# Kernel tuning notes

Hardware: AMD Instinct MI355X
Metric: run time of the kernel (lower is better)

Reference implementation:

```python
import jax, jax.numpy as jnp
import numpy as np

VOCAB = 21128; EMBED = 768; D_MODEL = 256; H = 100; NTAGS = 21; B = 32; T = 256


def setup_inputs() -> dict:
    key = jax.random.key(0)
    ks = jax.random.split(key, 18)
    n = lambda k, s, sc=0.05: jax.random.normal(k, s, dtype=jnp.float32) * sc
    return {
        "words": jax.random.randint(ks[0], (B, T), 0, VOCAB),
        "target": jax.random.randint(ks[1], (B, T), 0, NTAGS),
        "embed_table": n(ks[2], (VOCAB, EMBED), 1.0),
        "in_fc_w": n(ks[3], (D_MODEL, EMBED)),
        "in_fc_b": n(ks[4], (D_MODEL,)),
        "Wih0": n(ks[5], (2, 4 * H, D_MODEL)),
        "Whh0": n(ks[6], (2, 4 * H, H)),
        "bih0": n(ks[7], (2, 4 * H)),
        "bhh0": n(ks[8], (2, 4 * H)),
        "Wih1": n(ks[9], (2, 4 * H, 2 * H)),
        "Whh1": n(ks[10], (2, 4 * H, H)),
        "bih1": n(ks[11], (2, 4 * H)),
        "bhh1": n(ks[12], (2, 4 * H)),
        "out_w": n(ks[13], (NTAGS, 2 * H)),
        "out_b": n(ks[14], (NTAGS,)),
        "trans": n(ks[15], (NTAGS, NTAGS)),
        "start_s": n(ks[16], (NTAGS,)),
        "end_s": n(ks[17], (NTAGS,)),
    }


def _lstm_dir(x, Wih, Whh, bih, bhh, reverse):
    # x: (T, B, D); torch LSTM gate order i, f, g, o
    Bsz, Hd = x.shape[1], Whh.shape[1]
    pre = jnp.einsum('tbd,gd->tbg', x, Wih) + bih  # precompute input projection

    def step(carry, p):
        h, c = carry
        g = p + h @ Whh.T + bhh
        i, f, gg, o = jnp.split(g, 4, axis=-1)
        c = jax.nn.sigmoid(f) * c + jax.nn.sigmoid(i) * jnp.tanh(gg)
        h = jax.nn.sigmoid(o) * jnp.tanh(c)
        return (h, c), h

    init = (jnp.zeros((Bsz, Hd), x.dtype), jnp.zeros((Bsz, Hd), x.dtype))
    _, hs = jax.lax.scan(step, init, pre, reverse=reverse)
    return hs


def _bilstm(x, layers):
    h = x
    for (Wih, Whh, bih, bhh) in layers:  # fixed small loop over num_layers
        f = _lstm_dir(h, Wih[0], Whh[0], bih[0], bhh[0], False)
        b = _lstm_dir(h, Wih[1], Whh[1], bih[1], bhh[1], True)
        h = jnp.concatenate([f, b], axis=-1)
    return h


def _crf_loss(logits, tags, mask, trans, start_s, end_s):
    # fastNLP ConditionalRandomField loss: normalizer - gold_score, per batch elem
    lt = jnp.swapaxes(logits, 0, 1)          # (T, B, N)
    tt = tags.T                               # (T, B)
    mt = mask.T.astype(logits.dtype)          # (T, B)
    alpha0 = lt[0] + start_s

    def step(alpha, inp):
        emit, m = inp
        tmp = alpha[:, :, None] + trans[None] + emit[:, None, :]  # (B, N, N)
        new = jax.nn.logsumexp(tmp, axis=1)
        return jnp.where(m[:, None] > 0, new, alpha), None

    alpha, _ = jax.lax.scan(step, alpha0, (lt[1:], mt[1:]))
    normalizer = jax.nn.logsumexp(alpha + end_s, axis=1)  # (B,)

    emit_sc = jnp.take_along_axis(lt, tt[..., None], axis=2)[..., 0] * mt
    trans_sc = trans[tt[:-1], tt[1:]] * mt[1:]
    seq_lens = mask.sum(axis=1)
    last_idx = jnp.maximum(seq_lens - 1, 0)
    last_tags = tags[jnp.arange(tags.shape[0]), last_idx]
    gold = emit_sc.sum(0) + trans_sc.sum(0) + start_s[tt[0]] + end_s[last_tags]
    return normalizer - gold


def reference(words, target, embed_table, in_fc_w, in_fc_b, Wih0, Whh0, bih0, bhh0,
              Wih1, Whh1, bih1, bhh1, out_w, out_b, trans, start_s, end_s):
    mask = words != 0
    x = embed_table[words]                       # (B, T, E)
    x = x @ in_fc_w.T + in_fc_b                  # (B, T, D)
    x = jnp.swapaxes(x, 0, 1)                    # (T, B, D)
    h = _bilstm(x, [(Wih0, Whh0, bih0, bhh0), (Wih1, Whh1, bih1, bhh1)])
    h = jnp.swapaxes(h, 0, 1)                    # (B, T, 2H); dropout is identity at eval
    logits = jax.nn.log_softmax(h @ out_w.T + out_b, axis=-1)
    return _crf_loss(logits, target, mask, trans, start_s, end_s)  # (B,)
```

## Files before the change

### kernel.cpp

```cpp
#include <hip/hip_runtime.h>
#include <hip/hip_bf16.h>

#define VOCAB 21128
#define EMBED 768
#define DMODEL 256
#define HID 100
#define NTAGS 21
#define BB 32
#define TT 256
#define NTOK (BB*TT)

typedef float f32x4 __attribute__((ext_vector_type(4)));
typedef unsigned int u32x4 __attribute__((ext_vector_type(4)));
typedef short s16x8 __attribute__((ext_vector_type(8)));

__device__ __forceinline__ float sigm(float x) { return 1.0f / (1.0f + __expf(-x)); }
__device__ __forceinline__ float tanh_(float x) { return 2.0f / (1.0f + __expf(-2.0f * x)) - 1.0f; }

__device__ __forceinline__ unsigned int bfr(float x) {
    unsigned int u = __float_as_uint(x);
    return (u + 0x7fffu + ((u >> 16) & 1u)) >> 16;
}
__device__ __forceinline__ unsigned int bfpack(float lo, float hi) {
    return (bfr(hi) << 16) | bfr(lo);
}
__device__ __forceinline__ s16x8 asfrag(u32x4 v) {
    union { u32x4 u; s16x8 s; } x; x.u = v; return x.s;
}

__global__ __launch_bounds__(256) void gemm_mfma(
    const float* __restrict__ A, int lda,
    const float* __restrict__ B, int ldb,
    const float* __restrict__ bias1, const float* __restrict__ bias2,
    float* __restrict__ C, int ldc,
    int N, int K,
    const int* __restrict__ gatherWords, int permGates)
{
    __shared__ unsigned int As_[2][2048];
    __shared__ unsigned int Bs_[2][1024];

    const int tid = threadIdx.x;
    const int row0 = blockIdx.x * 128;
    const int col0 = blockIdx.y * 64;
    const int lane = tid & 63;
    const int wave = tid >> 6;
    const int wr = wave >> 1, wc = wave & 1;
    const int nsteps = (K + 31) >> 5;

    const float* arow[4]; int aoff[4]; int kqA[4];
    #pragma unroll
    for (int j = 0; j < 4; ++j) {
        int v = tid + 256 * j;
        int row = v >> 3, kq = v & 7;
        int grow = row0 + row;
        const float* ap;
        if (gatherWords) {
            int widx = gatherWords[(grow & 31) * TT + (grow >> 5)];
            ap = A + (size_t)widx * lda;
        } else {
            ap = A + (size_t)grow * lda;
        }
        arow[j] = ap + 4 * kq;
        aoff[j] = (row >> 4) * 256 + (kq >> 1) * 64 + (row & 15) * 4 + (kq & 1) * 2;
        kqA[j] = kq;
    }
    const float* brow[2]; int boff[2]; int bok[2]; int kqB[2];
    #pragma unroll
    for (int j = 0; j < 2; ++j) {
        int v = tid + 256 * j;
        int r = v >> 3, kq = v & 7;
        int gcol = col0 + r;
        bok[j] = (gcol < N);
        int src = bok[j] ? gcol : 0;
        if (permGates && bok[j]) {
            int d2 = (gcol >= 400) ? 1 : 0;
            int rr = gcol - d2 * 400;
            src = d2 * 400 + (rr & 3) * 100 + (rr >> 2);
        }
        brow[j] = B + (size_t)src * ldb + 4 * kq;
        boff[j] = (r >> 4) * 256 + (kq >> 1) * 64 + (r & 15) * 4 + (kq & 1) * 2;
        kqB[j] = kq;
    }

    {
        #pragma unroll
        for (int j = 0; j < 4; ++j) {
            f32x4 v = {0.f,0.f,0.f,0.f};
            if (4 * kqA[j] < K) v = *(const f32x4*)(arow[j]);
            As_[0][aoff[j]]     = bfpack(v.x, v.y);
            As_[0][aoff[j] + 1] = bfpack(v.z, v.w);
        }
        #pragma unroll
        for (int j = 0; j < 2; ++j) {
            f32x4 v = {0.f,0.f,0.f,0.f};
            if (bok[j] && 4 * kqB[j] < K) v = *(const f32x4*)(brow[j]);
            Bs_[0][boff[j]]     = bfpack(v.x, v.y);
            Bs_[0][boff[j] + 1] = bfpack(v.z, v.w);
        }
    }
    __syncthreads();

    f32x4 acc[4][2] = {};

    for (int s = 0; s < nsteps; ++s) {
        const int cur = s & 1, nxt = cur ^ 1;

        f32x4 la[4], lb[2];
        if (s + 1 < nsteps) {
            const int kb = (s + 1) * 32;
            #pragma unroll
            for (int j = 0; j < 4; ++j) {
                la[j] = (f32x4){0.f,0.f,0.f,0.f};
                if (kb + 4 * kqA[j] < K) la[j] = *(const f32x4*)(arow[j] + kb);
            }
            #pragma unroll
            for (int j = 0; j < 2; ++j) {
                lb[j] = (f32x4){0.f,0.f,0.f,0.f};
                if (bok[j] && kb + 4 * kqB[j] < K) lb[j] = *(const f32x4*)(brow[j] + kb);
            }
        }

        u32x4 af[4], bf[2];
        #pragma unroll
        for (int mt = 0; mt < 4; ++mt)
            af[mt] = *(const u32x4*)&As_[cur][(4 * wr + mt) * 256 + lane * 4];
        #pragma unroll
        for (int nt = 0; nt < 2; ++nt)
            bf[nt] = *(const u32x4*)&Bs_[cur][(2 * wc + nt) * 256 + lane * 4];
        #pragma unroll
        for (int mt = 0; mt < 4; ++mt)
            #pragma unroll
            for (int nt = 0; nt < 2; ++nt)
                acc[mt][nt] = __builtin_amdgcn_mfma_f32_16x16x32_bf16(
                    asfrag(af[mt]), asfrag(bf[nt]), acc[mt][nt], 0, 0, 0);

        if (s + 1 < nsteps) {
            #pragma unroll
            for (int j = 0; j < 4; ++j) {
                As_[nxt][aoff[j]]     = bfpack(la[j].x, la[j].y);
                As_[nxt][aoff[j] + 1] = bfpack(la[j].z, la[j].w);
            }
            #pragma unroll
            for (int j = 0; j < 2; ++j) {
                Bs_[nxt][boff[j]]     = bfpack(lb[j].x, lb[j].y);
                Bs_[nxt][boff[j] + 1] = bfpack(lb[j].z, lb[j].w);
            }
        }
        __syncthreads();
    }

    const int r4 = (lane >> 4) * 4;
    const int cl = lane & 15;
    #pragma unroll
    for (int nt = 0; nt < 2; ++nt) {
        int gcol = col0 + (2 * wc + nt) * 16 + cl;
        if (gcol < N) {
            int src = gcol;
            if (permGates) {
                int d2 = (gcol >= 400) ? 1 : 0;
                int rr = gcol - d2 * 400;
                src = d2 * 400 + (rr & 3) * 100 + (rr >> 2);
            }
            float bv = bias1[src];
            if (bias2) bv += bias2[src];
            #pragma unroll
            for (int mt = 0; mt < 4; ++mt) {
                int grow = row0 + (4 * wr + mt) * 16 + r4;
                #pragma unroll
                for (int r = 0; r < 4; ++r)
                    C[(size_t)(grow + r) * ldc + gcol] = acc[mt][nt][r] + bv;
            }
        }
    }
}

#define STASH_FRAG(DD, F, A0,A1,A2,A3) { \
    int tile = 4*wave + DD; if (tile > 24) tile = 24; \
    int row16 = 16*tile + m16; \
    const float* srcp = Whh + (size_t)(dir*400 + (row16 & 3)*100 + (row16 >> 2)) * HID; \
    const int k0 = 32*F + 8*g4; \
    f32x4 fa = {0.f,0.f,0.f,0.f}, fb = {0.f,0.f,0.f,0.f}; \
    if (k0 < HID) fa = *(const f32x4*)(srcp + k0); \
    if (k0 + 4 < HID) fb = *(const f32x4*)(srcp + k0 + 4); \
    unsigned p0 = bfpack(fa.x, fa.y), p1 = bfpack(fa.z, fa.w); \
    unsigned p2 = bfpack(fb.x, fb.y), p3 = bfpack(fb.z, fb.w); \
    asm volatile("v_accvgpr_write_b32 a" #A0 ", %0\n\t" \
                 "v_accvgpr_write_b32 a" #A1 ", %1\n\t" \
                 "v_accvgpr_write_b32 a" #A2 ", %2\n\t" \
                 "v_accvgpr_write_b32 a" #A3 ", %3" \
                 :: "v"(p0), "v"(p1), "v"(p2), "v"(p3) \
                 : "a" #A0, "a" #A1, "a" #A2, "a" #A3); }

#define MF(ACC, BF, A0, A3) \
    asm volatile("v_mfma_f32_16x16x32_bf16 %0, a[" #A0 ":" #A3 "], %1, %0" \
                 : "+v"(ACC) : "v"(BF));

#define LSTM_STEP(P0,P1,P2,P3, S) { \
    const int t_ = dir ? (TT-1-(S)) : (S); \
    const int i_ = t_ * BB + b; \
    const u32x4* hb_ = (const u32x4*)&h16[(S) & 1][0]; \
    u32x4 bf0 = hb_[g4], bf1 = hb_[4+g4], bf2 = hb_[8+g4], bf3 = hb_[12+g4]; \
    f32x4 acc0 = P0, acc1 = P1, acc2 = P2, acc3 = P3; \
    if ((S) + 2 < TT) { \
        const int tn_ = dir ? (TT-3-(S)) : ((S)+2); \
        const size_t ib_ = (size_t)(tn_ * BB + b) * 800; \
        P0 = *(const f32x4*)(pre + ib_ + po0); \
        P1 = *(const f32x4*)(pre + ib_ + po1); \
        P2 = *(const f32x4*)(pre + ib_ + po2); \
        P3 = *(const f32x4*)(pre + ib_ + po3); \
    } \
    asm volatile("s_nop 1"); \
    MF(acc0, bf0, 0, 3)   MF(acc1, bf0, 16, 19) MF(acc2, bf0, 32, 35) MF(acc3, bf0, 48, 51) \
    MF(acc0, bf1, 4, 7)   MF(acc1, bf1, 20, 23) MF(acc2, bf1, 36, 39) MF(acc3, bf1, 52, 55) \
    MF(acc0, bf2, 8, 11)  MF(acc1, bf2, 24, 27) MF(acc2, bf2, 40, 43) MF(acc3, bf2, 56, 59) \
    MF(acc0, bf3, 12, 15) MF(acc1, bf3, 28, 31) MF(acc2, bf3, 44, 47) MF(acc3, bf3, 60, 63) \
    asm volatile("s_nop 7\n\ts_nop 7"); \
    f32x4 sel = (d == 0) ? acc0 : (d == 1) ? acc1 : (d == 2) ? acc2 : acc3; \
    float igt = sigm(sel.x); \
    float fgt = sigm(sel.y); \
    float ggt = tanh_(sel.z); \
    float ogt = sigm(sel.w); \
    c = fgt * c + igt * ggt; \
    float h = ogt * tanh_(c); \
    if (writer) { \
        h16[((S) + 1) & 1][my_u] = (unsigned short)bfr(h); \
        hout[(size_t)i_ * 200 + dir * HID + my_u] = h; \
    } \
    __syncthreads(); }

__global__ __launch_bounds__(448, 1) void lstm_mfma(
    const float* __restrict__ pre,
    const float* __restrict__ Whh,
    float* __restrict__ hout)
{
    const int dir = blockIdx.x >> 5;
    const int b = blockIdx.x & 31;
    const int tid = threadIdx.x;
    const int wave = tid >> 6;
    const int lane = tid & 63;
    const int m16 = lane & 15;
    const int g4 = lane >> 4;
    const int d = lane & 3;

    __shared__ alignas(16) unsigned short h16[2][128];

    STASH_FRAG(0,0, 0,1,2,3)    STASH_FRAG(0,1, 4,5,6,7)
    STASH_FRAG(0,2, 8,9,10,11)  STASH_FRAG(0,3, 12,13,14,15)
    STASH_FRAG(1,0, 16,17,18,19) STASH_FRAG(1,1, 20,21,22,23)
    STASH_FRAG(1,2, 24,25,26,27) STASH_FRAG(1,3, 28,29,30,31)
    STASH_FRAG(2,0, 32,33,34,35) STASH_FRAG(2,1, 36,37,38,39)
    STASH_FRAG(2,2, 40,41,42,43) STASH_FRAG(2,3, 44,45,46,47)
    STASH_FRAG(3,0, 48,49,50,51) STASH_FRAG(3,1, 52,53,54,55)
    STASH_FRAG(3,2, 56,57,58,59) STASH_FRAG(3,3, 60,61,62,63)

    if (tid < 128) { h16[0][tid] = 0; h16[1][tid] = 0; }

    int tl0 = 4*wave + 0; if (tl0 > 24) tl0 = 24;
    int tl1 = 4*wave + 1; if (tl1 > 24) tl1 = 24;
    int tl2 = 4*wave + 2; if (tl2 > 24) tl2 = 24;
    int tl3 = 4*wave + 3; if (tl3 > 24) tl3 = 24;
    const int po0 = dir*400 + 16*tl0 + 4*g4;
    const int po1 = dir*400 + 16*tl1 + 4*g4;
    const int po2 = dir*400 + 16*tl2 + 4*g4;
    const int po3 = dir*400 + 16*tl3 + 4*g4;
    int my_tile = 4*wave + d; if (my_tile > 24) my_tile = 24;
    const int my_u = my_tile*4 + g4;
    const bool writer = ((lane & 12) == 0) && (wave < 6 || d == 0);

    float c = 0.f;
    __syncthreads();

    const size_t ib0 = (size_t)((dir ? (TT-1) : 0) * BB + b) * 800;
    const size_t ib1 = (size_t)((dir ? (TT-2) : 1) * BB + b) * 800;
    f32x4 pa0 = *(const f32x4*)(pre + ib0 + po0);
    f32x4 pa1 = *(const f32x4*)(pre + ib0 + po1);
    f32x4 pa2 = *(const f32x4*)(pre + ib0 + po2);
    f32x4 pa3 = *(const f32x4*)(pre + ib0 + po3);
    f32x4 pb0 = *(const f32x4*)(pre + ib1 + po0);
    f32x4 pb1 = *(const f32x4*)(pre + ib1 + po1);
    f32x4 pb2 = *(const f32x4*)(pre + ib1 + po2);
    f32x4 pb3 = *(const f32x4*)(pre + ib1 + po3);

    for (int s = 0; s < TT; s += 2) {
        LSTM_STEP(pa0, pa1, pa2, pa3, s)
        LSTM_STEP(pb0, pb1, pb2, pb3, s + 1)
    }
}

__global__ __launch_bounds__(256) void logits_lsm(
    const float* __restrict__ h1,
    const float* __restrict__ out_w,
    const float* __restrict__ out_b,
    float* __restrict__ logits)
{
    const int lane = threadIdx.x & 63;
    const int wid = (blockIdx.x * 256 + threadIdx.x) >> 6;
    const int half = lane >> 5;
    const int n = lane & 31;
    const int i = wid * 2 + half;
    if (i >= NTOK) return;

    float acc = -1e30f;
    if (n < NTAGS) {
        acc = out_b[n];
        const float4* hr = (const float4*)(h1 + (size_t)i * 200);
        const float4* wr = (const float4*)(out_w + (size_t)n * 200);
        #pragma unroll
        for (int e = 0; e < 50; ++e) {
            float4 h4 = hr[e], w4 = wr[e];
            acc += h4.x * w4.x + h4.y * w4.y + h4.z * w4.z + h4.w * w4.w;
        }
    }
    float m = acc;
    for (int off = 16; off > 0; off >>= 1) m = fmaxf(m, __shfl_xor(m, off, 32));
    float ex = (n < NTAGS) ? __expf(acc - m) : 0.f;
    float s = ex;
    for (int off = 16; off > 0; off >>= 1) s += __shfl_xor(s, off, 32);
    if (n < NTAGS) logits[(size_t)i * NTAGS + n] = acc - m - __logf(s);
}

__global__ __launch_bounds__(64) void crf_kernel(
    const float* __restrict__ logits,
    const int* __restrict__ words,
    const int* __restrict__ target,
    const float* __restrict__ trans,
    const float* __restrict__ start_s,
    const float* __restrict__ end_s,
    float* __restrict__ out)
{
    const int b = blockIdx.x;
    const int j = threadIdx.x;

    float tcol[NTAGS];
    #pragma unroll
    for (int i = 0; i < NTAGS; ++i) tcol[i] = (j < NTAGS) ? trans[i * NTAGS + j] : 0.f;

    float alpha = (j < NTAGS) ? (logits[(size_t)(0 * BB + b) * NTAGS + j] + start_s[j]) : -1e30f;

    for (int t = 1; t < TT; ++t) {
        bool mt = (words[b * TT + t] != 0);
        if (mt) {
            float v[NTAGS];
            float mx = -1e30f;
            #pragma unroll
            for (int i2 = 0; i2 < NTAGS; ++i2) {
                float ai = __shfl(alpha, i2, 64);
                v[i2] = ai + tcol[i2];
                mx = fmaxf(mx, v[i2]);
            }
            float s = 0.f;
            #pragma unroll
            for (int i2 = 0; i2 < NTAGS; ++i2) s += __expf(v[i2] - mx);
            float na = mx + __logf(s) + logits[(size_t)(t * BB + b) * NTAGS + j];
            alpha = (j < NTAGS) ? na : -1e30f;
        }
    }

    float val = (j < NTAGS) ? (alpha + end_s[j]) : -1e30f;
    float mx = val;
    for (int off = 32; off > 0; off >>= 1) mx = fmaxf(mx, __shfl_xor(mx, off, 64));
    float s = (j < NTAGS) ? __expf(val - mx) : 0.f;
    for (int off = 32; off > 0; off >>= 1) s += __shfl_xor(s, off, 64);
    float norm = mx + __logf(s);

    float gold = 0.f, slen = 0.f;
    for (int t = j; t < TT; t += 64) {
        int tg = target[b * TT + t];
        bool m = (words[b * TT + t] != 0);
        if (m) {
            gold += logits[(size_t)(t * BB + b) * NTAGS + tg];
            slen += 1.f;
            if (t >= 1) gold += trans[target[b * TT + t - 1] * NTAGS + tg];
        }
    }
    for (int off = 32; off > 0; off >>= 1) {
        gold += __shfl_xor(gold, off, 64);
        slen += __shfl_xor(slen, off, 64);
    }
    if (j == 0) {
        int len = (int)slen;
        int last = (len > 0) ? (len - 1) : 0;
        int last_tag = target[b * TT + last];
        gold += start_s[target[b * TT + 0]] + end_s[last_tag];
        out[b] = norm - gold;
    }
}

extern "C" void kernel_launch(void* const* d_in, const int* in_sizes, int n_in,
                              void* d_out, int out_size, void* d_ws, size_t ws_size,
                              hipStream_t stream) {
    const int*   words   = (const int*)  d_in[0];
    const int*   target  = (const int*)  d_in[1];
    const float* embed   = (const float*)d_in[2];
    const float* in_fc_w = (const float*)d_in[3];
    const float* in_fc_b = (const float*)d_in[4];
    const float* Wih0    = (const float*)d_in[5];
    const float* Whh0    = (const float*)d_in[6];
    const float* bih0    = (const float*)d_in[7];
    const float* bhh0    = (const float*)d_in[8];
    const float* Wih1    = (const float*)d_in[9];
    const float* Whh1    = (const float*)d_in[10];
    const float* bih1    = (const float*)d_in[11];
    const float* bhh1    = (const float*)d_in[12];
    const float* out_w   = (const float*)d_in[13];
    const float* out_b   = (const float*)d_in[14];
    const float* trans   = (const float*)d_in[15];
    const float* start_s = (const float*)d_in[16];
    const float* end_s   = (const float*)d_in[17];
    float* out = (float*)d_out;

    float* ws = (float*)d_ws;
    float* x      = ws;
    float* pre    = ws + 2097152;
    float* h0     = ws + 8650752;
    float* h1     = ws;
    float* logits = ws + 1638400;

    gemm_mfma<<<dim3(64, 4), 256, 0, stream>>>(
        embed, EMBED, in_fc_w, EMBED, in_fc_b, nullptr,
        x, DMODEL, DMODEL, EMBED, words, 0);

    gemm_mfma<<<dim3(64, 13), 256, 0, stream>>>(
        x, DMODEL, Wih0, DMODEL, bih0, bhh0,
        pre, 800, 800, DMODEL, nullptr, 1);

    lstm_mfma<<<64, 448, 0, stream>>>(pre, Whh0, h0);

    gemm_mfma<<<dim3(64, 13), 256, 0, stream>>>(
        h0, 200, Wih1, 200, bih1, bhh1,
        pre, 800, 800, 200, nullptr, 1);

    lstm_mfma<<<64, 448, 0, stream>>>(pre, Whh1, h1);

    logits_lsm<<<NTOK / 8, 256, 0, stream>>>(h1, out_w, out_b, logits);

    crf_kernel<<<BB, 64, 0, stream>>>(logits, words, target, trans, start_s, end_s, out);
}
```

Baseline: 619.0 us.

## Stage LSTM gate preactivations in LDS chunks and use lighter barriers

Result: faster. 580.6 us (-6.2%).

```diff
diff --git a/kernel.cpp b/kernel.cpp
--- a/kernel.cpp
+++ b/kernel.cpp
@@ -27,6 +27,12 @@
 __device__ __forceinline__ s16x8 asfrag(u32x4 v) {
     union { u32x4 u; s16x8 s; } x; x.u = v; return x.s;
 }
+
+#define BAR() do { \
+    asm volatile("s_waitcnt lgkmcnt(0)" ::: "memory"); \
+    __builtin_amdgcn_s_barrier(); \
+    __builtin_amdgcn_sched_barrier(0); \
+} while (0)
 
 __global__ __launch_bounds__(256) void gemm_mfma(
     const float* __restrict__ A, int lda,
@@ -98,7 +104,7 @@
             Bs_[0][boff[j] + 1] = bfpack(v.z, v.w);
         }
     }
-    __syncthreads();
+    BAR();
 
     f32x4 acc[4][2] = {};
 
@@ -146,7 +152,7 @@
                 Bs_[nxt][boff[j] + 1] = bfpack(lb[j].z, lb[j].w);
             }
         }
-        __syncthreads();
+        BAR();
     }
 
     const int r4 = (lane >> 4) * 4;
@@ -195,20 +201,29 @@
     asm volatile("v_mfma_f32_16x16x32_bf16 %0, a[" #A0 ":" #A3 "], %1, %0" \
                  : "+v"(ACC) : "v"(BF));
 
-#define LSTM_STEP(P0,P1,P2,P3, S) { \
-    const int t_ = dir ? (TT-1-(S)) : (S); \
-    const int i_ = t_ * BB + b; \
-    const u32x4* hb_ = (const u32x4*)&h16[(S) & 1][0]; \
+#define LOADCHUNK(K2) { \
+    const int s0_ = 16 * (K2); \
+    _Pragma("unroll") \
+    for (int j = 0; j < 4; ++j) { \
+        if (okj[j]) { \
+            int tg = dir ? (TT - 1 - (s0_ + sicj[j])) : (s0_ + sicj[j]); \
+            rr[j] = *(const f32x4*)(pre + (size_t)(tg * BB + b) * 800 + dir * 400 + 4 * gqj[j]); \
+        } \
+    } }
+
+#define WRITECHUNK(BUF) { \
+    _Pragma("unroll") \
+    for (int j = 0; j < 4; ++j) { \
+        if (okj[j]) *(f32x4*)&preS[(BUF) * 6400 + sicj[j] * 400 + 4 * gqj[j]] = rr[j]; \
+    } }
+
+#define LSTM_STEP(SIC) { \
+    const int t_ = dir ? (TT - 1 - (s0 + (SIC))) : (s0 + (SIC)); \
+    const u32x4* hb_ = (const u32x4*)&h16[(SIC) & 1][0]; \
     u32x4 bf0 = hb_[g4], bf1 = hb_[4+g4], bf2 = hb_[8+g4], bf3 = hb_[12+g4]; \
-    f32x4 acc0 = P0, acc1 = P1, acc2 = P2, acc3 = P3; \
-    if ((S) + 2 < TT) { \
-        const int tn_ = dir ? (TT-3-(S)) : ((S)+2); \
-        const size_t ib_ = (size_t)(tn_ * BB + b) * 800; \
-        P0 = *(const f32x4*)(pre + ib_ + po0); \
-        P1 = *(const f32x4*)(pre + ib_ + po1); \
-        P2 = *(const f32x4*)(pre + ib_ + po2); \
-        P3 = *(const f32x4*)(pre + ib_ + po3); \
-    } \
+    f32x4 p4 = *(const f32x4*)&preS[curbase + (SIC) * 400 + my_po]; \
+    f32x4 acc0 = {0.f,0.f,0.f,0.f}, acc1 = {0.f,0.f,0.f,0.f}; \
+    f32x4 acc2 = {0.f,0.f,0.f,0.f}, acc3 = {0.f,0.f,0.f,0.f}; \
     asm volatile("s_nop 1"); \
     MF(acc0, bf0, 0, 3)   MF(acc1, bf0, 16, 19) MF(acc2, bf0, 32, 35) MF(acc3, bf0, 48, 51) \
     MF(acc0, bf1, 4, 7)   MF(acc1, bf1, 20, 23) MF(acc2, bf1, 36, 39) MF(acc3, bf1, 52, 55) \
@@ -216,17 +231,17 @@
     MF(acc0, bf3, 12, 15) MF(acc1, bf3, 28, 31) MF(acc2, bf3, 44, 47) MF(acc3, bf3, 60, 63) \
     asm volatile("s_nop 7\n\ts_nop 7"); \
     f32x4 sel = (d == 0) ? acc0 : (d == 1) ? acc1 : (d == 2) ? acc2 : acc3; \
-    float igt = sigm(sel.x); \
-    float fgt = sigm(sel.y); \
-    float ggt = tanh_(sel.z); \
-    float ogt = sigm(sel.w); \
+    float igt = sigm(sel.x + p4.x); \
+    float fgt = sigm(sel.y + p4.y); \
+    float ggt = tanh_(sel.z + p4.z); \
+    float ogt = sigm(sel.w + p4.w); \
     c = fgt * c + igt * ggt; \
     float h = ogt * tanh_(c); \
     if (writer) { \
-        h16[((S) + 1) & 1][my_u] = (unsigned short)bfr(h); \
-        hout[(size_t)i_ * 200 + dir * HID + my_u] = h; \
+        h16[((SIC) + 1) & 1][my_u] = (unsigned short)bfr(h); \
+        hout[(size_t)(t_ * BB + b) * 200 + dir * HID + my_u] = h; \
     } \
-    __syncthreads(); }
+    BAR(); }
 
 __global__ __launch_bounds__(448, 1) void lstm_mfma(
     const float* __restrict__ pre,
@@ -243,6 +258,7 @@
     const int d = lane & 3;
 
     __shared__ alignas(16) unsigned short h16[2][128];
+    __shared__ alignas(16) float preS[2 * 6400];
 
     STASH_FRAG(0,0, 0,1,2,3)    STASH_FRAG(0,1, 4,5,6,7)
     STASH_FRAG(0,2, 8,9,10,11)  STASH_FRAG(0,3, 12,13,14,15)
@@ -255,35 +271,39 @@
 
     if (tid < 128) { h16[0][tid] = 0; h16[1][tid] = 0; }
 
-    int tl0 = 4*wave + 0; if (tl0 > 24) tl0 = 24;
-    int tl1 = 4*wave + 1; if (tl1 > 24) tl1 = 24;
-    int tl2 = 4*wave + 2; if (tl2 > 24) tl2 = 24;
-    int tl3 = 4*wave + 3; if (tl3 > 24) tl3 = 24;
-    const int po0 = dir*400 + 16*tl0 + 4*g4;
-    const int po1 = dir*400 + 16*tl1 + 4*g4;
-    const int po2 = dir*400 + 16*tl2 + 4*g4;
-    const int po3 = dir*400 + 16*tl3 + 4*g4;
-    int my_tile = 4*wave + d; if (my_tile > 24) my_tile = 24;
-    const int my_u = my_tile*4 + g4;
+    int my_tile = 4 * wave + d; if (my_tile > 24) my_tile = 24;
+    const int my_u = my_tile * 4 + g4;
+    const int my_po = 16 * my_tile + 4 * g4;
     const bool writer = ((lane & 12) == 0) && (wave < 6 || d == 0);
 
+    int sicj[4], gqj[4]; bool okj[4];
+    #pragma unroll
+    for (int j = 0; j < 4; ++j) {
+        int idx = tid + 448 * j;
+        okj[j] = (idx < 1600);
+        int ic = okj[j] ? idx : 0;
+        sicj[j] = ic / 100;
+        gqj[j] = ic - 100 * sicj[j];
+    }
+
     float c = 0.f;
-    __syncthreads();
-
-    const size_t ib0 = (size_t)((dir ? (TT-1) : 0) * BB + b) * 800;
-    const size_t ib1 = (size_t)((dir ? (TT-2) : 1) * BB + b) * 800;
-    f32x4 pa0 = *(const f32x4*)(pre + ib0 + po0);
-    f32x4 pa1 = *(const f32x4*)(pre + ib0 + po1);
-    f32x4 pa2 = *(const f32x4*)(pre + ib0 + po2);
-    f32x4 pa3 = *(const f32x4*)(pre + ib0 + po3);
-    f32x4 pb0 = *(const f32x4*)(pre + ib1 + po0);
-    f32x4 pb1 = *(const f32x4*)(pre + ib1 + po1);
-    f32x4 pb2 = *(const f32x4*)(pre + ib1 + po2);
-    f32x4 pb3 = *(const f32x4*)(pre + ib1 + po3);
-
-    for (int s = 0; s < TT; s += 2) {
-        LSTM_STEP(pa0, pa1, pa2, pa3, s)
-        LSTM_STEP(pb0, pb1, pb2, pb3, s + 1)
+    f32x4 rr[4];
+
+    LOADCHUNK(0)
+    WRITECHUNK(0)
+    LOADCHUNK(1)
+    BAR();
+
+    for (int k = 0; k < 16; ++k) {
+        const int s0 = 16 * k;
+        const int curbase = (k & 1) * 6400;
+        LSTM_STEP(0)  LSTM_STEP(1)  LSTM_STEP(2)  LSTM_STEP(3)
+        LSTM_STEP(4)  LSTM_STEP(5)  LSTM_STEP(6)  LSTM_STEP(7)
+        LSTM_STEP(8)  LSTM_STEP(9)  LSTM_STEP(10) LSTM_STEP(11)
+        LSTM_STEP(12) LSTM_STEP(13) LSTM_STEP(14) LSTM_STEP(15)
+        if (k < 15) { WRITECHUNK((k & 1) ^ 1) }
+        if (k < 14) { LOADCHUNK(k + 2) }
+        BAR();
     }
 }
 
```
